# Kernel optimization log

Hardware: AMD Instinct MI355X
Metric: run time of the kernel (lower is better)

## Reference

```python
import jax, jax.numpy as jnp
import numpy as np

MARGIN = 1.0
EPS = 1e-12


def setup_inputs() -> dict:
    key = jax.random.key(0)
    k1, k2, k3 = jax.random.split(key, 3)
    B, C, D = 16384, 500, 512
    features = jax.random.normal(k1, (B, D), dtype=jnp.float32)
    prototypes = jax.random.normal(k2, (C, D), dtype=jnp.float32)
    labels = jax.random.randint(k3, (B,), 0, C, dtype=jnp.int64)
    return {"features": features, "prototypes": prototypes, "labels": labels}


def reference(features, prototypes, labels):
    # Pairwise L2 distances [B, C] via the expanded form (no [B,C,D] intermediate)
    f2 = jnp.sum(features * features, axis=-1, keepdims=True)   # [B, 1]
    p2 = jnp.sum(prototypes * prototypes, axis=-1)               # [C]
    sq = f2 + p2 - 2.0 * (features @ prototypes.T)               # [B, C]
    dists = jnp.sqrt(jnp.maximum(sq, EPS))                       # [B, C]

    B, C = dists.shape
    d_pos = jnp.take_along_axis(dists, labels[:, None], axis=1)[:, 0]  # [B]
    pos_mask = jax.nn.one_hot(labels, C, dtype=bool)             # [B, C]
    d_neg_min = jnp.min(jnp.where(pos_mask, jnp.inf, dists), axis=-1)  # [B]

    loss = jnp.mean(jax.nn.relu(d_pos - d_neg_min + MARGIN))
    return loss
```

## Files before the change

### kernel.cpp

```cpp
#include <hip/hip_runtime.h>
#include <stdint.h>
#include <stddef.h>

#define BB 16384
#define CC 500
#define DD 512
#define PADC 512
#define LMARGIN 1.0f
#define EPSQ 1e-12f
#define NK 16

typedef __attribute__((ext_vector_type(8))) _Float16 f16x8;
typedef __attribute__((ext_vector_type(4))) float f32x4;

#define GLOBAL_AS __attribute__((address_space(1)))
#define LDS_AS __attribute__((address_space(3)))

__device__ __forceinline__ void ld_lds16(const void* g, void* l) {
  __builtin_amdgcn_global_load_lds((const GLOBAL_AS void*)g, (LDS_AS void*)l, 16, 0, 0);
}

__global__ void prepP_kernel(const float* __restrict__ protos,
                             unsigned short* __restrict__ protoH,
                             float* __restrict__ p2,
                             float* __restrict__ out) {
  int c = blockIdx.x * 4 + (threadIdx.x >> 6);
  int lane = threadIdx.x & 63;
  if (c == 0 && lane == 0) out[0] = 0.f;
  f32x4 a0 = {0.f, 0.f, 0.f, 0.f}, a1 = a0;
  if (c < CC) {
    const float* src = protos + (size_t)c * DD + lane * 8;
    a0 = *(const f32x4*)src;
    a1 = *(const f32x4*)(src + 4);
  }
  f16x8 h;
  float s = 0.f;
#pragma unroll
  for (int u = 0; u < 4; ++u) {
    h[u] = (_Float16)a0[u];
    h[u + 4] = (_Float16)a1[u];
    s = fmaf(a0[u], a0[u], s);
    s = fmaf(a1[u], a1[u], s);
  }
  *(f16x8*)(protoH + (size_t)c * DD + lane * 8) = h;
#pragma unroll
  for (int d = 1; d < 64; d <<= 1) s += __shfl_xor(s, d, 64);
  if (lane == 0) p2[c] = s;
}

__global__ void prepF_kernel(const float* __restrict__ feat,
                             unsigned short* __restrict__ featH,
                             float* __restrict__ f2) {
  int row = blockIdx.x * 4 + (threadIdx.x >> 6);
  int lane = threadIdx.x & 63;
  const float* src = feat + (size_t)row * DD + lane * 8;
  f32x4 a0 = *(const f32x4*)src;
  f32x4 a1 = *(const f32x4*)(src + 4);
  f16x8 h;
  float s = 0.f;
#pragma unroll
  for (int u = 0; u < 4; ++u) {
    h[u] = (_Float16)a0[u];
    h[u + 4] = (_Float16)a1[u];
    s = fmaf(a0[u], a0[u], s);
    s = fmaf(a1[u], a1[u], s);
  }
  *(f16x8*)(featH + (size_t)row * DD + lane * 8) = h;
#pragma unroll
  for (int d = 1; d < 64; d <<= 1) s += __shfl_xor(s, d, 64);
  if (lane == 0) f2[row] = s;
}

__launch_bounds__(256, 2)
__global__ void gemm_kernel(const unsigned short* __restrict__ featH,
                            const unsigned short* __restrict__ protoH,
                            const float* __restrict__ f2,
                            const float* __restrict__ p2,
                            const int* __restrict__ labels,
                            float2* __restrict__ ws2) {
  __shared__ __align__(16) unsigned short Ab[2][128 * 32];
  __shared__ __align__(16) unsigned short Bb[2][128 * 32];
  __shared__ float f2l[128], p2l[128];
  __shared__ int labl[128];
  __shared__ float redM[2][128], redP[2][128];

  const int tid = threadIdx.x;
  const int w = tid >> 6;
  const int lane = tid & 63;
  const int lane16 = lane & 15;
  const int quad = lane >> 4;
  const int wm = w & 1;
  const int wn = w >> 1;
  const int r0 = blockIdx.x * 128;
  const int c0 = blockIdx.y * 128;

  const int srow = w * 16 + (lane >> 2);
  const int sbyte = (lane & 3) * 16;
  const char* gA = (const char*)featH + ((size_t)(r0 + srow) * DD) * 2 + sbyte;
  const char* gB = (const char*)protoH + ((size_t)(c0 + srow) * DD) * 2 + sbyte;

#define STAGE(kc, buf)                                                       \
  do {                                                                       \
    char* lA = (char*)&Ab[buf][0] + w * 1024 + lane * 16;                    \
    char* lB = (char*)&Bb[buf][0] + w * 1024 + lane * 16;                    \
    ld_lds16(gA + (kc) * 64, lA);                                            \
    ld_lds16(gA + (kc) * 64 + (size_t)64 * DD * 2, lA + 4096);               \
    ld_lds16(gB + (kc) * 64, lB);                                            \
    ld_lds16(gB + (kc) * 64 + (size_t)64 * DD * 2, lB + 4096);               \
  } while (0)

  STAGE(0, 0);

  if (tid < 128) {
    f2l[tid] = f2[r0 + tid];
    p2l[tid] = p2[c0 + tid];
    labl[tid] = labels[r0 + tid];
  }

  f32x4 acc[4][4];
#pragma unroll
  for (int ms = 0; ms < 4; ++ms)
#pragma unroll
    for (int ns = 0; ns < 4; ++ns) acc[ms][ns] = (f32x4){0.f, 0.f, 0.f, 0.f};

  __syncthreads();

  int buf = 0;
  for (int kc = 0; kc < NK; ++kc) {
    if (kc + 1 < NK) STAGE(kc + 1, buf ^ 1);

    f16x8 af[4], bfr[4];
#pragma unroll
    for (int ms = 0; ms < 4; ++ms)
      af[ms] = *(const f16x8*)(&Ab[buf][(wm * 64 + ms * 16 + lane16) * 32 +
                                        quad * 8]);
#pragma unroll
    for (int ns = 0; ns < 4; ++ns)
      bfr[ns] = *(const f16x8*)(&Bb[buf][(wn * 64 + ns * 16 + lane16) * 32 +
                                         quad * 8]);
#pragma unroll
    for (int ms = 0; ms < 4; ++ms)
#pragma unroll
      for (int ns = 0; ns < 4; ++ns)
        acc[ms][ns] = __builtin_amdgcn_mfma_f32_16x16x32_f16(
            af[ms], bfr[ns], acc[ms][ns], 0, 0, 0);

    __syncthreads();
    buf ^= 1;
  }

#pragma unroll
  for (int ms = 0; ms < 4; ++ms) {
#pragma unroll
    for (int i = 0; i < 4; ++i) {
      const int rowIn = wm * 64 + ms * 16 + quad * 4 + i;
      const float f2v = f2l[rowIn];
      const int lb = labl[rowIn];
      float m = 1e30f, p = -1e30f;
#pragma unroll
      for (int ns = 0; ns < 4; ++ns) {
        const int colIn = wn * 64 + ns * 16 + lane16;
        const int col = c0 + colIn;
        float d = sqrtf(fmaxf(f2v + p2l[colIn] - 2.f * acc[ms][ns][i], EPSQ));
        bool isPos = (col == lb);
        p = fmaxf(p, isPos ? d : -1e30f);
        m = fminf(m, (!isPos && col < CC) ? d : 1e30f);
      }
#pragma unroll
      for (int d = 1; d < 16; d <<= 1) {
        m = fminf(m, __shfl_xor(m, d, 64));
        p = fmaxf(p, __shfl_xor(p, d, 64));
      }
      if (lane16 == 0) {
        redM[wn][rowIn] = m;
        redP[wn][rowIn] = p;
      }
    }
  }
  __syncthreads();

  if (tid < 128) {
    float m = fminf(redM[0][tid], redM[1][tid]);
    float p = fmaxf(redP[0][tid], redP[1][tid]);
    ws2[(size_t)(r0 + tid) * 4 + blockIdx.y] = make_float2(m, p);
  }
#undef STAGE
}

__global__ void reduce_kernel(const float2* __restrict__ ws2,
                              float* __restrict__ out) {
  int row = blockIdx.x * 256 + threadIdx.x;
  const float4* v = (const float4*)ws2;
  float4 a = v[(size_t)row * 2];
  float4 b = v[(size_t)row * 2 + 1];
  float m = fminf(fminf(a.x, a.z), fminf(b.x, b.z));
  float p = fmaxf(fmaxf(a.y, a.w), fmaxf(b.y, b.w));
  float term = fmaxf(p - m + LMARGIN, 0.f);
#pragma unroll
  for (int d = 1; d < 64; d <<= 1) term += __shfl_xor(term, d, 64);
  __shared__ float ws4[4];
  if ((threadIdx.x & 63) == 0) ws4[threadIdx.x >> 6] = term;
  __syncthreads();
  if (threadIdx.x == 0)
    atomicAdd(out, (ws4[0] + ws4[1] + ws4[2] + ws4[3]) * (1.0f / BB));
}

extern "C" void kernel_launch(void* const* d_in, const int* in_sizes, int n_in,
                              void* d_out, int out_size, void* d_ws, size_t ws_size,
                              hipStream_t stream) {
  const float* feat = (const float*)d_in[0];
  const float* protos = (const float*)d_in[1];
  const int* labels = (const int*)d_in[2];
  float* out = (float*)d_out;

  char* ws = (char*)d_ws;
  unsigned short* protoH = (unsigned short*)(ws);
  unsigned short* featH = (unsigned short*)(ws + (1 << 20));
  float* p2 = (float*)(ws + (17 << 20));
  float* f2 = (float*)(ws + (17 << 20) + (4 << 10));
  float2* ws2 = (float2*)(ws + (17 << 20) + (128 << 10));

  prepP_kernel<<<PADC / 4, 256, 0, stream>>>(protos, protoH, p2, out);
  prepF_kernel<<<BB / 4, 256, 0, stream>>>(feat, featH, f2);
  dim3 grid(BB / 128, PADC / 128);
  gemm_kernel<<<grid, 256, 0, stream>>>(featH, protoH, f2, p2, labels, ws2);
  reduce_kernel<<<BB / 256, 256, 0, stream>>>(ws2, out);
}
```

Measured before the change: 101.4 us.

## Fuse feature fp16 conversion, GEMM, and loss reduction into one kernel

```diff
diff --git a/kernel.cpp b/kernel.cpp
--- a/kernel.cpp
+++ b/kernel.cpp
@@ -11,6 +11,7 @@
 #define NK 16
 
 typedef __attribute__((ext_vector_type(8))) _Float16 f16x8;
+typedef __attribute__((ext_vector_type(4))) _Float16 f16x4;
 typedef __attribute__((ext_vector_type(4))) float f32x4;
 
 #define GLOBAL_AS __attribute__((address_space(1)))
@@ -48,120 +49,125 @@
   if (lane == 0) p2[c] = s;
 }
 
-__global__ void prepF_kernel(const float* __restrict__ feat,
-                             unsigned short* __restrict__ featH,
-                             float* __restrict__ f2) {
-  int row = blockIdx.x * 4 + (threadIdx.x >> 6);
-  int lane = threadIdx.x & 63;
-  const float* src = feat + (size_t)row * DD + lane * 8;
-  f32x4 a0 = *(const f32x4*)src;
-  f32x4 a1 = *(const f32x4*)(src + 4);
-  f16x8 h;
-  float s = 0.f;
-#pragma unroll
-  for (int u = 0; u < 4; ++u) {
-    h[u] = (_Float16)a0[u];
-    h[u + 4] = (_Float16)a1[u];
-    s = fmaf(a0[u], a0[u], s);
-    s = fmaf(a1[u], a1[u], s);
-  }
-  *(f16x8*)(featH + (size_t)row * DD + lane * 8) = h;
-#pragma unroll
-  for (int d = 1; d < 64; d <<= 1) s += __shfl_xor(s, d, 64);
-  if (lane == 0) f2[row] = s;
-}
-
-__launch_bounds__(256, 2)
-__global__ void gemm_kernel(const unsigned short* __restrict__ featH,
+__launch_bounds__(512, 2)
+__global__ void main_kernel(const float* __restrict__ feat,
                             const unsigned short* __restrict__ protoH,
-                            const float* __restrict__ f2,
                             const float* __restrict__ p2,
                             const int* __restrict__ labels,
-                            float2* __restrict__ ws2) {
-  __shared__ __align__(16) unsigned short Ab[2][128 * 32];
-  __shared__ __align__(16) unsigned short Bb[2][128 * 32];
-  __shared__ float f2l[128], p2l[128];
-  __shared__ int labl[128];
-  __shared__ float redM[2][128], redP[2][128];
+                            float* __restrict__ out) {
+  __shared__ __align__(16) unsigned short Bb[2][PADC * 32];
+  __shared__ __align__(16) unsigned short Ab[2][64 * 32];
+  __shared__ float p2l[PADC];
+  __shared__ float f2l[64];
+  __shared__ int labl[64];
+  __shared__ float redM[4][64], redP[4][64];
 
   const int tid = threadIdx.x;
   const int w = tid >> 6;
   const int lane = tid & 63;
   const int lane16 = lane & 15;
   const int quad = lane >> 4;
-  const int wm = w & 1;
-  const int wn = w >> 1;
-  const int r0 = blockIdx.x * 128;
-  const int c0 = blockIdx.y * 128;
-
-  const int srow = w * 16 + (lane >> 2);
-  const int sbyte = (lane & 3) * 16;
-  const char* gA = (const char*)featH + ((size_t)(r0 + srow) * DD) * 2 + sbyte;
-  const char* gB = (const char*)protoH + ((size_t)(c0 + srow) * DD) * 2 + sbyte;
-
-#define STAGE(kc, buf)                                                       \
-  do {                                                                       \
-    char* lA = (char*)&Ab[buf][0] + w * 1024 + lane * 16;                    \
-    char* lB = (char*)&Bb[buf][0] + w * 1024 + lane * 16;                    \
-    ld_lds16(gA + (kc) * 64, lA);                                            \
-    ld_lds16(gA + (kc) * 64 + (size_t)64 * DD * 2, lA + 4096);               \
-    ld_lds16(gB + (kc) * 64, lB);                                            \
-    ld_lds16(gB + (kc) * 64 + (size_t)64 * DD * 2, lB + 4096);               \
-  } while (0)
-
-  STAGE(0, 0);
-
-  if (tid < 128) {
-    f2l[tid] = f2[r0 + tid];
-    p2l[tid] = p2[c0 + tid];
-    labl[tid] = labels[r0 + tid];
-  }
-
-  f32x4 acc[4][4];
-#pragma unroll
-  for (int ms = 0; ms < 4; ++ms)
-#pragma unroll
-    for (int ns = 0; ns < 4; ++ns) acc[ms][ns] = (f32x4){0.f, 0.f, 0.f, 0.f};
+  const int mh = w & 1;
+  const int nq = w >> 1;
+  const int r0 = blockIdx.x * 64;
+
+  const int arow = tid >> 3;
+  const int akoff = (tid & 7) * 4;
+  const float* aSrc = feat + (size_t)(r0 + arow) * DD + akoff;
+
+  const char* pB = (const char*)protoH;
+  const char* bSrc[4];
+  int bDst[4];
+#pragma unroll
+  for (int j = 0; j < 4; ++j) {
+    int col = (w * 4 + j) * 16 + (lane >> 2);
+    bSrc[j] = pB + (size_t)col * (DD * 2) + (lane & 3) * 16;
+    bDst[j] = (w * 4 + j) * 1024 + lane * 16;
+  }
+
+#pragma unroll
+  for (int j = 0; j < 4; ++j) ld_lds16(bSrc[j], (char*)&Bb[0][0] + bDst[j]);
+
+  float f2acc = 0.f;
+  {
+    f32x4 a = *(const f32x4*)aSrc;
+    f16x4 h;
+#pragma unroll
+    for (int u = 0; u < 4; ++u) {
+      h[u] = (_Float16)a[u];
+      f2acc = fmaf(a[u], a[u], f2acc);
+    }
+    *(f16x4*)(&Ab[0][arow * 32 + akoff]) = h;
+  }
+  p2l[tid] = p2[tid];
+  if (tid < 64) labl[tid] = labels[r0 + tid];
+
+  f32x4 acc[2][8];
+#pragma unroll
+  for (int ms = 0; ms < 2; ++ms)
+#pragma unroll
+    for (int ns = 0; ns < 8; ++ns) acc[ms][ns] = (f32x4){0.f, 0.f, 0.f, 0.f};
 
   __syncthreads();
 
   int buf = 0;
   for (int kc = 0; kc < NK; ++kc) {
-    if (kc + 1 < NK) STAGE(kc + 1, buf ^ 1);
-
-    f16x8 af[4], bfr[4];
-#pragma unroll
-    for (int ms = 0; ms < 4; ++ms)
-      af[ms] = *(const f16x8*)(&Ab[buf][(wm * 64 + ms * 16 + lane16) * 32 +
+    f32x4 aNext;
+    if (kc + 1 < NK) {
+#pragma unroll
+      for (int j = 0; j < 4; ++j)
+        ld_lds16(bSrc[j] + (kc + 1) * 64, (char*)&Bb[buf ^ 1][0] + bDst[j]);
+      aNext = *(const f32x4*)(aSrc + (kc + 1) * 32);
+    }
+
+    f16x8 af[2], bfr[8];
+#pragma unroll
+    for (int ms = 0; ms < 2; ++ms)
+      af[ms] = *(const f16x8*)(&Ab[buf][(mh * 32 + ms * 16 + lane16) * 32 +
                                         quad * 8]);
 #pragma unroll
-    for (int ns = 0; ns < 4; ++ns)
-      bfr[ns] = *(const f16x8*)(&Bb[buf][(wn * 64 + ns * 16 + lane16) * 32 +
+    for (int ns = 0; ns < 8; ++ns)
+      bfr[ns] = *(const f16x8*)(&Bb[buf][(nq * 128 + ns * 16 + lane16) * 32 +
                                          quad * 8]);
 #pragma unroll
-    for (int ms = 0; ms < 4; ++ms)
-#pragma unroll
-      for (int ns = 0; ns < 4; ++ns)
+    for (int ms = 0; ms < 2; ++ms)
+#pragma unroll
+      for (int ns = 0; ns < 8; ++ns)
         acc[ms][ns] = __builtin_amdgcn_mfma_f32_16x16x32_f16(
             af[ms], bfr[ns], acc[ms][ns], 0, 0, 0);
 
+    if (kc + 1 < NK) {
+      f16x4 h;
+#pragma unroll
+      for (int u = 0; u < 4; ++u) {
+        h[u] = (_Float16)aNext[u];
+        f2acc = fmaf(aNext[u], aNext[u], f2acc);
+      }
+      *(f16x4*)(&Ab[buf ^ 1][arow * 32 + akoff]) = h;
+    }
+
     __syncthreads();
     buf ^= 1;
   }
 
-#pragma unroll
-  for (int ms = 0; ms < 4; ++ms) {
+  f2acc += __shfl_xor(f2acc, 1, 64);
+  f2acc += __shfl_xor(f2acc, 2, 64);
+  f2acc += __shfl_xor(f2acc, 4, 64);
+  if ((tid & 7) == 0) f2l[arow] = f2acc;
+  __syncthreads();
+
+#pragma unroll
+  for (int ms = 0; ms < 2; ++ms) {
 #pragma unroll
     for (int i = 0; i < 4; ++i) {
-      const int rowIn = wm * 64 + ms * 16 + quad * 4 + i;
+      const int rowIn = mh * 32 + ms * 16 + quad * 4 + i;
       const float f2v = f2l[rowIn];
       const int lb = labl[rowIn];
       float m = 1e30f, p = -1e30f;
 #pragma unroll
-      for (int ns = 0; ns < 4; ++ns) {
-        const int colIn = wn * 64 + ns * 16 + lane16;
-        const int col = c0 + colIn;
-        float d = sqrtf(fmaxf(f2v + p2l[colIn] - 2.f * acc[ms][ns][i], EPSQ));
+      for (int ns = 0; ns < 8; ++ns) {
+        const int col = nq * 128 + ns * 16 + lane16;
+        float d = sqrtf(fmaxf(f2v + p2l[col] - 2.f * acc[ms][ns][i], EPSQ));
         bool isPos = (col == lb);
         p = fmaxf(p, isPos ? d : -1e30f);
         m = fminf(m, (!isPos && col < CC) ? d : 1e30f);
@@ -172,37 +178,23 @@
         p = fmaxf(p, __shfl_xor(p, d, 64));
       }
       if (lane16 == 0) {
-        redM[wn][rowIn] = m;
-        redP[wn][rowIn] = p;
+        redM[nq][rowIn] = m;
+        redP[nq][rowIn] = p;
       }
     }
   }
   __syncthreads();
 
-  if (tid < 128) {
-    float m = fminf(redM[0][tid], redM[1][tid]);
-    float p = fmaxf(redP[0][tid], redP[1][tid]);
-    ws2[(size_t)(r0 + tid) * 4 + blockIdx.y] = make_float2(m, p);
-  }
-#undef STAGE
-}
-
-__global__ void reduce_kernel(const float2* __restrict__ ws2,
-                              float* __restrict__ out) {
-  int row = blockIdx.x * 256 + threadIdx.x;
-  const float4* v = (const float4*)ws2;
-  float4 a = v[(size_t)row * 2];
-  float4 b = v[(size_t)row * 2 + 1];
-  float m = fminf(fminf(a.x, a.z), fminf(b.x, b.z));
-  float p = fmaxf(fmaxf(a.y, a.w), fmaxf(b.y, b.w));
-  float term = fmaxf(p - m + LMARGIN, 0.f);
-#pragma unroll
-  for (int d = 1; d < 64; d <<= 1) term += __shfl_xor(term, d, 64);
-  __shared__ float ws4[4];
-  if ((threadIdx.x & 63) == 0) ws4[threadIdx.x >> 6] = term;
-  __syncthreads();
-  if (threadIdx.x == 0)
-    atomicAdd(out, (ws4[0] + ws4[1] + ws4[2] + ws4[3]) * (1.0f / BB));
+  if (tid < 64) {
+    float m = fminf(fminf(redM[0][tid], redM[1][tid]),
+                    fminf(redM[2][tid], redM[3][tid]));
+    float p = fmaxf(fmaxf(redP[0][tid], redP[1][tid]),
+                    fmaxf(redP[2][tid], redP[3][tid]));
+    float term = fmaxf(p - m + LMARGIN, 0.f);
+#pragma unroll
+    for (int d = 1; d < 64; d <<= 1) term += __shfl_xor(term, d, 64);
+    if (tid == 0) atomicAdd(out, term * (1.0f / BB));
+  }
 }
 
 extern "C" void kernel_launch(void* const* d_in, const int* in_sizes, int n_in,
@@ -215,14 +207,8 @@
 
   char* ws = (char*)d_ws;
   unsigned short* protoH = (unsigned short*)(ws);
-  unsigned short* featH = (unsigned short*)(ws + (1 << 20));
-  float* p2 = (float*)(ws + (17 << 20));
-  float* f2 = (float*)(ws + (17 << 20) + (4 << 10));
-  float2* ws2 = (float2*)(ws + (17 << 20) + (128 << 10));
+  float* p2 = (float*)(ws + (1 << 20));
 
   prepP_kernel<<<PADC / 4, 256, 0, stream>>>(protos, protoH, p2, out);
-  prepF_kernel<<<BB / 4, 256, 0, stream>>>(feat, featH, f2);
-  dim3 grid(BB / 128, PADC / 128);
-  gemm_kernel<<<grid, 256, 0, stream>>>(featH, protoH, f2, p2, labels, ws2);
-  reduce_kernel<<<BB / 256, 256, 0, stream>>>(ws2, out);
-}
+  main_kernel<<<BB / 64, 512, 0, stream>>>(feat, protoH, p2, labels, out);
+}
```

Measured after the change: 99.75 us. No clear change (-1.6%).
